# Kernel optimization log

Hardware: AMD Instinct MI355X
Metric: run time of the kernel (lower is better)

Reference implementation:

```python
import jax, jax.numpy as jnp
import numpy as np

N_NODES = 100000
N_EDGES = 1600000
HIDDEN = 64
LEAKY_SLOPE = 0.01  # torch F.leaky_relu default


def setup_inputs() -> dict:
    key = jax.random.key(0)
    k1, k2, k3, k4 = jax.random.split(key, 4)
    x = jax.random.normal(k1, (N_NODES, HIDDEN), dtype=jnp.float32)
    edge_index = jax.random.randint(k2, (2, N_EDGES), 0, N_NODES, dtype=jnp.int64)
    # Linear(hidden, 1, bias=False) weights, squeezed to [hidden]
    w_i = jax.random.normal(k3, (HIDDEN,), dtype=jnp.float32) * 0.1
    w_j = jax.random.normal(k4, (HIDDEN,), dtype=jnp.float32) * 0.1
    return {"x": x, "edge_index": edge_index, "w_i": w_i, "w_j": w_j}


def reference(x, edge_index, w_i, w_j):
    n = x.shape[0]
    ej, ei = edge_index[0], edge_index[1]  # (edge_index_j, edge_index_i)
    # per-node attention scores, then per-edge gather
    s_i = x @ w_i  # [N]
    s_j = x @ w_j  # [N]
    e = jax.nn.leaky_relu(s_i[ei] + s_j[ej], LEAKY_SLOPE)  # [E]
    # segment softmax over edges grouped by destination node ei
    emax = jax.ops.segment_max(e, ei, num_segments=n)  # [N]
    ex = jnp.exp(e - emax[ei])  # [E]
    denom = jax.ops.segment_sum(ex, ei, num_segments=n)  # [N]
    alpha = ex / denom[ei]  # [E]
    # spmm: out[i] = sum_{edges e: dst=i} alpha_e * x[src_e]
    out = jax.ops.segment_sum(alpha[:, None] * x[ej], ei, num_segments=n)  # [N, H]
    return jax.nn.relu(out)
```

## Files before the change

### kernel.cpp

```cpp
#include <hip/hip_runtime.h>
#include <stdint.h>

#define N_NODES 100000
#define N_EDGES 1600000
#define HIDDEN  64
#define SLOPE   0.01f
#define NBUCK   782
#define CAPB    2816
#define PCHUNK  16384
#define NPART   98
#define NSB     391
#define NCAP    49


__device__ __forceinline__ unsigned short f2bf(float f) {
    uint32_t u = __float_as_uint(f);
    uint32_t r = u + 0x7FFFu + ((u >> 16) & 1u);
    return (unsigned short)(r >> 16);
}

__global__ void __launch_bounds__(1024) k_build(const float* __restrict__ x,
                                                const float* __restrict__ w_i,
                                                const float* __restrict__ w_j,
                                                const int* __restrict__ srcs,
                                                const int* __restrict__ dsts,
                                                float* __restrict__ s_i,
                                                float* __restrict__ s_j,
                                                unsigned short* __restrict__ xb,
                                                int* __restrict__ ctrl,
                                                uint32_t* __restrict__ pairs) {
    __shared__ int lcnt[NBUCK], lloc[NBUCK], lbase[NBUCK];
    __shared__ int scan[1024];
    __shared__ uint32_t srec[PCHUNK];
    int tid = threadIdx.x;
    if (blockIdx.x < NPART) {
        if (blockIdx.x == 0) {
            if (tid < NBUCK) atomicExch(&ctrl[tid], 0);
            __syncthreads();
            if (tid == 0) { __threadfence(); atomicExch(&ctrl[NBUCK], 1); }
        }
        if (tid < NBUCK) lcnt[tid] = 0;
        __syncthreads();
        int e0 = blockIdx.x * PCHUNK;
        int e1 = min(e0 + PCHUNK, N_EDGES);
        for (int e = e0 + tid; e < e1; e += 1024)
            atomicAdd(&lcnt[dsts[e] >> 7], 1);
        __syncthreads();
        int v = (tid < NBUCK) ? lcnt[tid] : 0;
        scan[tid] = v;
        __syncthreads();
        for (int off = 1; off < 1024; off <<= 1) {
            int t = (tid >= off) ? scan[tid - off] : 0;
            __syncthreads();
            scan[tid] += t;
            __syncthreads();
        }
        if (tid < NBUCK) lloc[tid] = scan[tid] - v;
        if (tid == 0)
            while (atomicAdd(&ctrl[NBUCK], 0) != 1) {}
        __syncthreads();
        if (tid < NBUCK) {
            lbase[tid] = v ? atomicAdd(&ctrl[tid], v) : 0;
            lcnt[tid] = 0;
        }
        __syncthreads();
        for (int e = e0 + tid; e < e1; e += 1024) {
            int src = srcs[e];
            int dst = dsts[e];
            int b = dst >> 7;
            int r = atomicAdd(&lcnt[b], 1);
            srec[lloc[b] + r] = ((uint32_t)(dst & 127) << 24) | (uint32_t)src;
        }
        __syncthreads();
        int wv = tid >> 6, ln = tid & 63;
        for (int b = wv; b < NBUCK; b += 16) {
            int c = lcnt[b];
            int lo = lloc[b], go = lbase[b];
            for (int j = ln; j < c; j += 64) {
                int pos = go + j;
                if (pos < CAPB)
                    pairs[(size_t)b * CAPB + pos] = srec[lo + j];
            }
        }
        return;
    }
    int u0 = blockIdx.x - NPART;
    int g16 = tid >> 4;
    int ql = tid & 15;
    float4 wi4 = ((const float4*)w_i)[ql];
    float4 wj4 = ((const float4*)w_j)[ql];
#pragma unroll
    for (int i = 0; i < 4; ++i) {
        int node = u0 * 256 + i * 64 + g16;
        if (node >= N_NODES) break;
        float4 v = ((const float4*)x)[node * 16 + ql];
        float a = v.x * wi4.x + v.y * wi4.y + v.z * wi4.z + v.w * wi4.w;
        float b = v.x * wj4.x + v.y * wj4.y + v.z * wj4.z + v.w * wj4.w;
#pragma unroll
        for (int off = 1; off < 16; off <<= 1) {
            a += __shfl_xor(a, off, 64);
            b += __shfl_xor(b, off, 64);
        }
        if (ql == 0) { s_i[node] = a; s_j[node] = b; }
        ushort4 o;
        o.x = f2bf(v.x); o.y = f2bf(v.y); o.z = f2bf(v.z); o.w = f2bf(v.w);
        ((ushort4*)xb)[node * 16 + ql] = o;
    }
}

__device__ __forceinline__ float bflo(uint32_t d) { return __uint_as_float(d << 16); }
__device__ __forceinline__ float bfhi(uint32_t d) { return __uint_as_float(d & 0xFFFF0000u); }

__global__ void __launch_bounds__(1024, 8) k_bucket_agg(const uint2* __restrict__ xw2,
                                                        const uint32_t* __restrict__ pairs,
                                                        const int* __restrict__ ctrl,
                                                        const float* __restrict__ s_i,
                                                        const float* __restrict__ s_j,
                                                        float* __restrict__ out) {
    __shared__ uint64_t spairs[128 * NCAP];
    __shared__ int lcur[128];
    __shared__ float s_si[128];
    int tid = threadIdx.x;
    int cb = blockIdx.x;
    int node0 = cb * 128;
    const uint32_t* reg = pairs + (size_t)cb * CAPB;
    int rcnt = min(ctrl[cb], CAPB);
    if (tid < 128) {
        lcur[tid] = 0;
        int node = node0 + tid;
        s_si[tid] = (node < N_NODES) ? s_i[node] : 0.f;
    }
    __syncthreads();
    for (int e = tid; e < rcnt; e += 1024) {
        uint32_t p = reg[e];
        int n = (int)(p >> 24);
        int src = (int)(p & 0xFFFFFFu);
        float sc = s_si[n] + s_j[src];
        sc = (sc > 0.f) ? sc : SLOPE * sc;
        float w = __expf(sc);
        int slot = atomicAdd(&lcur[n], 1);
        if (slot < NCAP)
            spairs[n * NCAP + slot] =
                ((uint64_t)__float_as_uint(w) << 32) | (uint32_t)src;
    }
    __syncthreads();
    int wave = tid >> 6, lane = tid & 63;
    int quarter = lane >> 4, ql = lane & 15;
    for (int half = 0; half < 2; ++half) {
        int k = wave * 4 + quarter + 64 * half;
        int node = node0 + k;
        int creal = lcur[k];
        int cq = min(creal, NCAP);
        int mx = cq;
        mx = max(mx, __shfl_xor(mx, 16, 64));
        mx = max(mx, __shfl_xor(mx, 32, 64));
        const uint64_t* pp = spairs + k * NCAP;
        float acc0 = 0.f, acc1 = 0.f, acc2 = 0.f, acc3 = 0.f, den = 0.f;
        for (int j = 0; j < mx; j += 4) {
            uint64_t qv[4];
#pragma unroll
            for (int u = 0; u < 4; ++u) {
                int idx = j + u;
                qv[u] = pp[(idx < cq) ? idx : 0];
            }
            uint2 d[4];
            float wv[4];
#pragma unroll
            for (int u = 0; u < 4; ++u) {
                int idx = j + u;
                uint32_t src = (idx < cq) ? ((uint32_t)qv[u] & 0xFFFFFFu) : 0u;
                wv[u] = (idx < cq) ? __uint_as_float((uint32_t)(qv[u] >> 32)) : 0.f;
                d[u] = xw2[src * 16 + ql];
            }
#pragma unroll
            for (int u = 0; u < 4; ++u) {
                float w = wv[u];
                den += w;
                acc0 = fmaf(w, bflo(d[u].x), acc0);
                acc1 = fmaf(w, bfhi(d[u].x), acc1);
                acc2 = fmaf(w, bflo(d[u].y), acc2);
                acc3 = fmaf(w, bfhi(d[u].y), acc3);
            }
        }
        if (creal > NCAP) {
            acc0 = acc1 = acc2 = acc3 = 0.f; den = 0.f;
            for (int e = 0; e < rcnt; ++e) {
                uint32_t p = reg[e];
                if ((int)(p >> 24) == k) {
                    int src = (int)(p & 0xFFFFFFu);
                    float sc = s_si[k] + s_j[src];
                    sc = (sc > 0.f) ? sc : SLOPE * sc;
                    float w = __expf(sc);
                    uint2 dd = xw2[(uint32_t)src * 16 + ql];
                    den += w;
                    acc0 = fmaf(w, bflo(dd.x), acc0);
                    acc1 = fmaf(w, bfhi(dd.x), acc1);
                    acc2 = fmaf(w, bflo(dd.y), acc2);
                    acc3 = fmaf(w, bfhi(dd.y), acc3);
                }
            }
        }
        if (node < N_NODES) {
            float4 r = make_float4(0.f, 0.f, 0.f, 0.f);
            if (creal > 0) {
                float inv = 1.f / den;
                r.x = fmaxf(acc0 * inv, 0.f);
                r.y = fmaxf(acc1 * inv, 0.f);
                r.z = fmaxf(acc2 * inv, 0.f);
                r.w = fmaxf(acc3 * inv, 0.f);
            }
            ((float4*)(out + (size_t)node * HIDDEN))[ql] = r;
        }
    }
}

extern "C" void kernel_launch(void* const* d_in, const int* in_sizes, int n_in,
                              void* d_out, int out_size, void* d_ws, size_t ws_size,
                              hipStream_t stream) {
    const float* x   = (const float*)d_in[0];
    const int*   ei  = (const int*)d_in[1];
    const float* w_i = (const float*)d_in[2];
    const float* w_j = (const float*)d_in[3];
    float* out = (float*)d_out;

    char* p = (char*)d_ws;
    float*          s_i   = (float*)p;          p += (size_t)N_NODES * 4;
    float*          s_j   = (float*)p;          p += (size_t)N_NODES * 4;
    unsigned short* xb    = (unsigned short*)p; p += (size_t)N_NODES * HIDDEN * 2;
    int*            ctrl  = (int*)p;            p += 4096;
    uint32_t*       pairs = (uint32_t*)p;

    const int* srcs = ei;
    const int* dsts = ei + N_EDGES;

    k_build     <<<NPART + NSB, 1024, 0, stream>>>(x, w_i, w_j, srcs, dsts,
                                                   s_i, s_j, xb, ctrl, pairs);
    k_bucket_agg<<<NBUCK, 1024, 0, stream>>>((const uint2*)xb, pairs, ctrl,
                                             s_i, s_j, out);
}
```

Before: 145.3 us.

## Split 16-lane node group into two 8-lane halves with 16-byte row gathers

The aggregation kernel now has each 16-lane group split into two 8-lane halves. Each half processes alternate edges and loads 16-byte bf16 chunks per lane, so a whole 128-byte row is fetched by 8 lanes. The halves are combined with a cross-lane shuffle before the output is written. The shared pair table is zero-filled and padded to a stride of 50, which removes the per-slot bounds predication, but per-node capacity drops to 48 so more high-degree nodes take the slow rescan path. The edge-scoring loop is also partially unrolled so the first two s_j gathers are issued together.

```diff
diff --git a/kernel.cpp b/kernel.cpp
--- a/kernel.cpp
+++ b/kernel.cpp
@@ -10,7 +10,8 @@
 #define PCHUNK  16384
 #define NPART   98
 #define NSB     391
-#define NCAP    49
+#define NCAP    48
+#define NSTRIDE 50
 
 
 __device__ __forceinline__ unsigned short f2bf(float f) {
@@ -111,13 +112,13 @@
 __device__ __forceinline__ float bflo(uint32_t d) { return __uint_as_float(d << 16); }
 __device__ __forceinline__ float bfhi(uint32_t d) { return __uint_as_float(d & 0xFFFF0000u); }
 
-__global__ void __launch_bounds__(1024, 8) k_bucket_agg(const uint2* __restrict__ xw2,
+__global__ void __launch_bounds__(1024, 8) k_bucket_agg(const uint4* __restrict__ xw4,
                                                         const uint32_t* __restrict__ pairs,
                                                         const int* __restrict__ ctrl,
                                                         const float* __restrict__ s_i,
                                                         const float* __restrict__ s_j,
                                                         float* __restrict__ out) {
-    __shared__ uint64_t spairs[128 * NCAP];
+    __shared__ uint64_t spairs[128 * NSTRIDE];
     __shared__ int lcur[128];
     __shared__ float s_si[128];
     int tid = threadIdx.x;
@@ -125,91 +126,135 @@
     int node0 = cb * 128;
     const uint32_t* reg = pairs + (size_t)cb * CAPB;
     int rcnt = min(ctrl[cb], CAPB);
+    for (int i = tid; i < 128 * NSTRIDE; i += 1024) spairs[i] = 0ull;
     if (tid < 128) {
         lcur[tid] = 0;
         int node = node0 + tid;
         s_si[tid] = (node < N_NODES) ? s_i[node] : 0.f;
     }
     __syncthreads();
-    for (int e = tid; e < rcnt; e += 1024) {
-        uint32_t p = reg[e];
-        int n = (int)(p >> 24);
-        int src = (int)(p & 0xFFFFFFu);
-        float sc = s_si[n] + s_j[src];
-        sc = (sc > 0.f) ? sc : SLOPE * sc;
-        float w = __expf(sc);
-        int slot = atomicAdd(&lcur[n], 1);
-        if (slot < NCAP)
-            spairs[n * NCAP + slot] =
-                ((uint64_t)__float_as_uint(w) << 32) | (uint32_t)src;
+    {
+        int e0 = tid, e1 = tid + 1024;
+        bool a0 = e0 < rcnt, a1 = e1 < rcnt;
+        uint32_t p0 = a0 ? reg[e0] : 0u;
+        uint32_t p1 = a1 ? reg[e1] : 0u;
+        float sj0 = a0 ? s_j[p0 & 0xFFFFFFu] : 0.f;
+        float sj1 = a1 ? s_j[p1 & 0xFFFFFFu] : 0.f;
+        if (a0) {
+            int n = (int)(p0 >> 24);
+            float sc = s_si[n] + sj0;
+            sc = (sc > 0.f) ? sc : SLOPE * sc;
+            float w = __expf(sc);
+            int slot = atomicAdd(&lcur[n], 1);
+            if (slot < NCAP)
+                spairs[n * NSTRIDE + slot] =
+                    ((uint64_t)__float_as_uint(w) << 32) | (p0 & 0xFFFFFFu);
+        }
+        if (a1) {
+            int n = (int)(p1 >> 24);
+            float sc = s_si[n] + sj1;
+            sc = (sc > 0.f) ? sc : SLOPE * sc;
+            float w = __expf(sc);
+            int slot = atomicAdd(&lcur[n], 1);
+            if (slot < NCAP)
+                spairs[n * NSTRIDE + slot] =
+                    ((uint64_t)__float_as_uint(w) << 32) | (p1 & 0xFFFFFFu);
+        }
+        for (int e = tid + 2048; e < rcnt; e += 1024) {
+            uint32_t p = reg[e];
+            int n = (int)(p >> 24);
+            float sc = s_si[n] + s_j[p & 0xFFFFFFu];
+            sc = (sc > 0.f) ? sc : SLOPE * sc;
+            float w = __expf(sc);
+            int slot = atomicAdd(&lcur[n], 1);
+            if (slot < NCAP)
+                spairs[n * NSTRIDE + slot] =
+                    ((uint64_t)__float_as_uint(w) << 32) | (p & 0xFFFFFFu);
+        }
     }
     __syncthreads();
     int wave = tid >> 6, lane = tid & 63;
-    int quarter = lane >> 4, ql = lane & 15;
-    for (int half = 0; half < 2; ++half) {
-        int k = wave * 4 + quarter + 64 * half;
+    int quarter = (lane >> 4) & 3;
+    int half8 = (lane >> 3) & 1;
+    int l8 = lane & 7;
+    for (int hl = 0; hl < 2; ++hl) {
+        int k = wave * 4 + quarter + 64 * hl;
         int node = node0 + k;
         int creal = lcur[k];
         int cq = min(creal, NCAP);
         int mx = cq;
         mx = max(mx, __shfl_xor(mx, 16, 64));
         mx = max(mx, __shfl_xor(mx, 32, 64));
-        const uint64_t* pp = spairs + k * NCAP;
-        float acc0 = 0.f, acc1 = 0.f, acc2 = 0.f, acc3 = 0.f, den = 0.f;
-        for (int j = 0; j < mx; j += 4) {
-            uint64_t qv[4];
-#pragma unroll
-            for (int u = 0; u < 4; ++u) {
-                int idx = j + u;
-                qv[u] = pp[(idx < cq) ? idx : 0];
-            }
-            uint2 d[4];
-            float wv[4];
-#pragma unroll
-            for (int u = 0; u < 4; ++u) {
-                int idx = j + u;
-                uint32_t src = (idx < cq) ? ((uint32_t)qv[u] & 0xFFFFFFu) : 0u;
-                wv[u] = (idx < cq) ? __uint_as_float((uint32_t)(qv[u] >> 32)) : 0.f;
-                d[u] = xw2[src * 16 + ql];
-            }
-#pragma unroll
-            for (int u = 0; u < 4; ++u) {
-                float w = wv[u];
+        const uint64_t* pp = spairs + k * NSTRIDE;
+        float acc[8] = {0.f, 0.f, 0.f, 0.f, 0.f, 0.f, 0.f, 0.f};
+        float den = 0.f;
+        for (int j = 0; j < mx; j += 8) {
+            uint64_t rec[4];
+            uint4 d[4];
+#pragma unroll
+            for (int t = 0; t < 4; ++t)
+                rec[t] = pp[j + 2 * t + half8];
+#pragma unroll
+            for (int t = 0; t < 4; ++t)
+                d[t] = xw4[((uint32_t)rec[t] & 0xFFFFFFu) * 8 + l8];
+#pragma unroll
+            for (int t = 0; t < 4; ++t) {
+                float w = __uint_as_float((uint32_t)(rec[t] >> 32));
                 den += w;
-                acc0 = fmaf(w, bflo(d[u].x), acc0);
-                acc1 = fmaf(w, bfhi(d[u].x), acc1);
-                acc2 = fmaf(w, bflo(d[u].y), acc2);
-                acc3 = fmaf(w, bfhi(d[u].y), acc3);
+                acc[0] = fmaf(w, bflo(d[t].x), acc[0]);
+                acc[1] = fmaf(w, bfhi(d[t].x), acc[1]);
+                acc[2] = fmaf(w, bflo(d[t].y), acc[2]);
+                acc[3] = fmaf(w, bfhi(d[t].y), acc[3]);
+                acc[4] = fmaf(w, bflo(d[t].z), acc[4]);
+                acc[5] = fmaf(w, bfhi(d[t].z), acc[5]);
+                acc[6] = fmaf(w, bflo(d[t].w), acc[6]);
+                acc[7] = fmaf(w, bfhi(d[t].w), acc[7]);
             }
         }
         if (creal > NCAP) {
-            acc0 = acc1 = acc2 = acc3 = 0.f; den = 0.f;
+#pragma unroll
+            for (int i = 0; i < 8; ++i) acc[i] = 0.f;
+            den = 0.f;
             for (int e = 0; e < rcnt; ++e) {
                 uint32_t p = reg[e];
                 if ((int)(p >> 24) == k) {
-                    int src = (int)(p & 0xFFFFFFu);
+                    uint32_t src = p & 0xFFFFFFu;
                     float sc = s_si[k] + s_j[src];
                     sc = (sc > 0.f) ? sc : SLOPE * sc;
-                    float w = __expf(sc);
-                    uint2 dd = xw2[(uint32_t)src * 16 + ql];
+                    float w = (half8 == 0) ? __expf(sc) : 0.f;
+                    uint4 dd = xw4[src * 8 + l8];
                     den += w;
-                    acc0 = fmaf(w, bflo(dd.x), acc0);
-                    acc1 = fmaf(w, bfhi(dd.x), acc1);
-                    acc2 = fmaf(w, bflo(dd.y), acc2);
-                    acc3 = fmaf(w, bfhi(dd.y), acc3);
+                    acc[0] = fmaf(w, bflo(dd.x), acc[0]);
+                    acc[1] = fmaf(w, bfhi(dd.x), acc[1]);
+                    acc[2] = fmaf(w, bflo(dd.y), acc[2]);
+                    acc[3] = fmaf(w, bfhi(dd.y), acc[3]);
+                    acc[4] = fmaf(w, bflo(dd.z), acc[4]);
+                    acc[5] = fmaf(w, bfhi(dd.z), acc[5]);
+                    acc[6] = fmaf(w, bflo(dd.w), acc[6]);
+                    acc[7] = fmaf(w, bfhi(dd.w), acc[7]);
                 }
             }
         }
-        if (node < N_NODES) {
-            float4 r = make_float4(0.f, 0.f, 0.f, 0.f);
+#pragma unroll
+        for (int i = 0; i < 8; ++i) acc[i] += __shfl_xor(acc[i], 8, 64);
+        den += __shfl_xor(den, 8, 64);
+        if (half8 == 0 && node < N_NODES) {
+            float4 r0 = make_float4(0.f, 0.f, 0.f, 0.f);
+            float4 r1 = r0;
             if (creal > 0) {
                 float inv = 1.f / den;
-                r.x = fmaxf(acc0 * inv, 0.f);
-                r.y = fmaxf(acc1 * inv, 0.f);
-                r.z = fmaxf(acc2 * inv, 0.f);
-                r.w = fmaxf(acc3 * inv, 0.f);
-            }
-            ((float4*)(out + (size_t)node * HIDDEN))[ql] = r;
+                r0.x = fmaxf(acc[0] * inv, 0.f);
+                r0.y = fmaxf(acc[1] * inv, 0.f);
+                r0.z = fmaxf(acc[2] * inv, 0.f);
+                r0.w = fmaxf(acc[3] * inv, 0.f);
+                r1.x = fmaxf(acc[4] * inv, 0.f);
+                r1.y = fmaxf(acc[5] * inv, 0.f);
+                r1.z = fmaxf(acc[6] * inv, 0.f);
+                r1.w = fmaxf(acc[7] * inv, 0.f);
+            }
+            float4* op = (float4*)(out + (size_t)node * HIDDEN + l8 * 8);
+            op[0] = r0;
+            op[1] = r1;
         }
     }
 }
@@ -235,6 +280,6 @@
 
     k_build     <<<NPART + NSB, 1024, 0, stream>>>(x, w_i, w_j, srcs, dsts,
                                                    s_i, s_j, xb, ctrl, pairs);
-    k_bucket_agg<<<NBUCK, 1024, 0, stream>>>((const uint2*)xb, pairs, ctrl,
+    k_bucket_agg<<<NBUCK, 1024, 0, stream>>>((const uint4*)xb, pairs, ctrl,
                                              s_i, s_j, out);
 }
```

Measured after the change: 143.2 us. No clear change (-1.4%).
